# Optimization experiments

Hardware: AMD Instinct MI355X
Metric: run time of the kernel (lower is better)

The kernel has to match this reference:

```python
import jax, jax.numpy as jnp
import numpy as np

N_CLIN = 38
N_PIX = 36
N_NODES = N_CLIN + N_PIX  # 74
FV = 128
B = 1024
HID = 512
N_OUT = 1


def _base_edges():
    # Faithful to Network.get_edges: self-edges for all nodes, then for each
    # pixel node i, bidirectional edges to every clinical node.
    ids = np.arange(N_NODES)
    parts = [np.stack([ids, ids])]
    c = np.arange(N_CLIN)
    for i in range(N_CLIN, N_NODES):
        ii = np.full(N_CLIN, i)
        parts.append(np.stack([ii, c]))
        parts.append(np.stack([c, ii]))
    return np.concatenate(parts, axis=1)  # (2, 2810)


def setup_inputs() -> dict:
    key = jax.random.key(0)
    ks = jax.random.split(key, 10)
    base = _base_edges()  # (2, E0)
    # Batched edge index: per-sample copy offset by ind*N_NODES (batch-major order,
    # matching the torch.cat loop).
    offs = np.arange(B)[None, :, None] * N_NODES  # (1, B, 1)
    edge_index = (base[:, None, :] + offs).reshape(2, -1)  # (2, B*E0)
    s = 1.0 / np.sqrt(FV)
    return {
        "clinical_embeddings": jax.random.normal(ks[0], (B, N_CLIN, FV), jnp.float32),
        "image_embeddings": jax.random.normal(ks[1], (B, N_PIX, FV), jnp.float32),
        # RMRM graph-net params (single message-passing layer, fv_dim -> fv_dim)
        "W_self": jax.random.normal(ks[2], (FV, FV), jnp.float32) * s,
        "W_msg": jax.random.normal(ks[3], (FV, FV), jnp.float32) * s,
        "b_g": jnp.zeros((FV,), jnp.float32),
        # OutputBlock MLP params: fv_dim*(n_clinical+1)=4992 -> 512 -> 1
        "W1": jax.random.normal(ks[4], (FV * (N_CLIN + 1), HID), jnp.float32) * (1.0 / np.sqrt(FV * (N_CLIN + 1))),
        "b1": jnp.zeros((HID,), jnp.float32),
        "W2": jax.random.normal(ks[5], (HID, N_OUT), jnp.float32) * (1.0 / np.sqrt(HID)),
        "b2": jnp.zeros((N_OUT,), jnp.float32),
        "edge_index": jnp.asarray(edge_index, jnp.int32),
    }


def reference(clinical_embeddings, image_embeddings, W_self, W_msg, b_g, W1, b1, W2, b2, edge_index):
    # Assemble node features: [B, n_nodes, fv] -> flat [B*n_nodes, fv]
    x = jnp.concatenate([clinical_embeddings, image_embeddings], axis=1)
    x = x.reshape(-1, FV)
    src, dst = edge_index[0], edge_index[1]
    n_total = B * N_NODES
    # Mean-aggregated message passing (RMRM layer): gather + segment-sum
    msg = jax.ops.segment_sum(x[src], dst, num_segments=n_total)  # [B*N, FV]
    deg = jax.ops.segment_sum(jnp.ones_like(src, jnp.float32), dst, num_segments=n_total)
    agg = msg / deg[:, None]
    h = jax.nn.relu(x @ W_self + agg @ W_msg + b_g)  # [B*N, FV]
    h = h.reshape(B, N_NODES, FV)
    graph_fvs_c = h[:, :N_CLIN]          # [B, 38, FV]
    graph_fvs_i = h[:, N_CLIN:]          # [B, 36, FV]
    # AvgPool2d(6,6) over [B, FV, 6, 6] == mean over the 36 pixel nodes
    gap = graph_fvs_i.mean(axis=1)       # [B, FV]
    combined = jnp.concatenate([graph_fvs_c, gap[:, None, :]], axis=1).reshape(B, -1)
    # OutputBlock MLP
    out = jax.nn.relu(combined @ W1 + b1) @ W2 + b2  # [B, 1]
    return out
```

## Files before the change

### kernel.cpp

```cpp
#include <hip/hip_runtime.h>

#define FV 128
#define NCLIN 38
#define NPIX 36
#define NTOT 74
#define BATCH 1024
#define HID 512
#define COMB 4992
#define XPAD 136

typedef __attribute__((ext_vector_type(4))) float f32x4;
typedef __attribute__((ext_vector_type(8))) short s16x8;

#define WS_WCT  0
#define WS_WIT  8192
#define WS_COMB 16384
#define WS_W1T  2572288
#define WS_Z    3850240

__device__ __forceinline__ unsigned short bf16_rne(float f) {
    union { float f; unsigned int u; } v; v.f = f;
    unsigned int u = v.u;
    u += 0x7fffu + ((u >> 16) & 1u);
    return (unsigned short)(u >> 16);
}
__device__ __forceinline__ float bf2f(unsigned short h) {
    union { unsigned int u; float f; } v; v.u = ((unsigned int)h) << 16;
    return v.f;
}

__global__ __launch_bounds__(256) void k_static(
    const float* __restrict__ W1, const float* __restrict__ wself,
    const float* __restrict__ wmsg, float* __restrict__ ws)
{
    const int t = threadIdx.x;
    if (blockIdx.x == 78) {
        unsigned short* WcT = (unsigned short*)(ws + WS_WCT);
        unsigned short* WiT = (unsigned short*)(ws + WS_WIT);
        const int r  = blockIdx.y * 16 + (t >> 4);
        const int f0 = (t & 15) * 8;
#pragma unroll
        for (int j = 0; j < 8; ++j) {
            const int f = f0 + j;
            const int idx = r * 128 + f;
            const float wm = wmsg[idx];
            const float s  = wself[idx];
            WcT[f * 128 + r] = bf16_rne(s + wm * (1.0f / 37.0f));
            WiT[f * 128 + r] = bf16_rne(s + wm * (1.0f / 39.0f));
        }
        return;
    }
    unsigned short* W1T = (unsigned short*)(ws + WS_W1T);
    const int k0 = blockIdx.x * 64;
    const int n0 = blockIdx.y * 64;
    __shared__ float tile[64][65];
    const int r16 = t >> 4;
    const int c4  = (t & 15) * 4;
#pragma unroll
    for (int p = 0; p < 4; ++p) {
        const int r = p * 16 + r16;
        const float4 v = *(const float4*)&W1[(size_t)(k0 + r) * HID + n0 + c4];
        tile[r][c4 + 0] = v.x; tile[r][c4 + 1] = v.y;
        tile[r][c4 + 2] = v.z; tile[r][c4 + 3] = v.w;
    }
    __syncthreads();
    const int j  = t >> 2;
    const int i0 = (t & 3) * 16;
    unsigned short tmp[16];
#pragma unroll
    for (int s = 0; s < 16; ++s) tmp[s] = bf16_rne(tile[i0 + s][j]);
    unsigned short* dst = &W1T[(size_t)(n0 + j) * COMB + k0 + i0];
    *(uint4*)&dst[0] = *(uint4*)&tmp[0];
    *(uint4*)&dst[8] = *(uint4*)&tmp[8];
}

__global__ __launch_bounds__(256) void k_batch(
    const float* __restrict__ clin, const float* __restrict__ img,
    const float* __restrict__ wmsg, const float* __restrict__ bg,
    float* __restrict__ ws)
{
    const int b = blockIdx.x;
    const int t = threadIdx.x;

    __shared__ __align__(16) unsigned short xl[NTOT * XPAD];
    __shared__ float lc[128];
    __shared__ float li[128];
    __shared__ float tcv[128];
    __shared__ float tiv[128];

    const float* xc = clin + (size_t)b * NCLIN * FV;
    const float* xi = img  + (size_t)b * NPIX * FV;
    for (int i = t; i < NCLIN * 32; i += 256) {
        const int row = i >> 5, c4 = (i & 31) * 4;
        const float4 v = *(const float4*)&xc[row * 128 + c4];
        ushort4 u;
        u.x = bf16_rne(v.x); u.y = bf16_rne(v.y);
        u.z = bf16_rne(v.z); u.w = bf16_rne(v.w);
        *(ushort4*)&xl[row * XPAD + c4] = u;
    }
    for (int i = t; i < NPIX * 32; i += 256) {
        const int row = i >> 5, c4 = (i & 31) * 4;
        const float4 v = *(const float4*)&xi[row * 128 + c4];
        ushort4 u;
        u.x = bf16_rne(v.x); u.y = bf16_rne(v.y);
        u.z = bf16_rne(v.z); u.w = bf16_rne(v.w);
        *(ushort4*)&xl[(NCLIN + row) * XPAD + c4] = u;
    }
    __syncthreads();

    const int f = t & 127;
    if (t < 128) {
        float s = 0.f;
#pragma unroll
        for (int n = 0; n < NCLIN; ++n) s += bf2f(xl[n * XPAD + f]);
        lc[f] = s * (1.0f / 39.0f);
    } else {
        float s = 0.f;
#pragma unroll
        for (int n = 0; n < NPIX; ++n) s += bf2f(xl[(NCLIN + n) * XPAD + f]);
        li[f] = s * (1.0f / 37.0f);
    }
    __syncthreads();

    {
        const float* src = (t < 128) ? li : lc;
        float acc = bg[f];
#pragma unroll 4
        for (int k = 0; k < 128; ++k) acc += src[k] * wmsg[k * 128 + f];
        if (t < 128) tcv[f] = acc; else tiv[f] = acc;
    }
    __syncthreads();

    const unsigned short* WcT = (const unsigned short*)(ws + WS_WCT);
    const unsigned short* WiT = (const unsigned short*)(ws + WS_WIT);
    unsigned short* combined =
        (unsigned short*)(ws + WS_COMB) + (size_t)b * COMB;

    const int wave = t >> 6;
    const int lane = t & 63;
    const int l16  = lane & 15;
    const int q    = lane >> 4;
    const int n0   = wave * 32 + l16;

#pragma unroll
    for (int phase = 0; phase < 2; ++phase) {
        const int NN   = phase ? NPIX : NCLIN;
        const int xoff = phase ? NCLIN : 0;
        const unsigned short* WT = phase ? WiT : WcT;
        const float* tvv = phase ? tiv : tcv;

        const int r0 = xoff + ((l16      < NN) ? l16      : (NN - 1));
        const int r1 = xoff + ((16 + l16 < NN) ? 16 + l16 : (NN - 1));
        const int r2 = xoff + ((32 + l16 < NN) ? 32 + l16 : (NN - 1));

        f32x4 acc[3][2] = {};
#pragma unroll
        for (int kk = 0; kk < 4; ++kk) {
            const int ko = kk * 32 + q * 8;
            const s16x8 a0 = *(const s16x8*)&xl[r0 * XPAD + ko];
            const s16x8 a1 = *(const s16x8*)&xl[r1 * XPAD + ko];
            const s16x8 a2 = *(const s16x8*)&xl[r2 * XPAD + ko];
            const s16x8 b0 = *(const s16x8*)&WT[(n0)      * 128 + ko];
            const s16x8 b1 = *(const s16x8*)&WT[(n0 + 16) * 128 + ko];
            acc[0][0] = __builtin_amdgcn_mfma_f32_16x16x32_bf16(a0, b0, acc[0][0], 0, 0, 0);
            acc[0][1] = __builtin_amdgcn_mfma_f32_16x16x32_bf16(a0, b1, acc[0][1], 0, 0, 0);
            acc[1][0] = __builtin_amdgcn_mfma_f32_16x16x32_bf16(a1, b0, acc[1][0], 0, 0, 0);
            acc[1][1] = __builtin_amdgcn_mfma_f32_16x16x32_bf16(a1, b1, acc[1][1], 0, 0, 0);
            acc[2][0] = __builtin_amdgcn_mfma_f32_16x16x32_bf16(a2, b0, acc[2][0], 0, 0, 0);
            acc[2][1] = __builtin_amdgcn_mfma_f32_16x16x32_bf16(a2, b1, acc[2][1], 0, 0, 0);
        }

        const float t0 = tvv[wave * 32 + l16];
        const float t1 = tvv[wave * 32 + 16 + l16];

        if (phase == 0) {
#pragma unroll
            for (int rt = 0; rt < 3; ++rt) {
#pragma unroll
                for (int r = 0; r < 4; ++r) {
                    const int node = rt * 16 + q * 4 + r;
                    if (node < NCLIN) {
                        combined[node * 128 + wave * 32 + l16] =
                            bf16_rne(fmaxf(acc[rt][0][r] + t0, 0.f));
                        combined[node * 128 + wave * 32 + 16 + l16] =
                            bf16_rne(fmaxf(acc[rt][1][r] + t1, 0.f));
                    }
                }
            }
        } else {
            float g0 = 0.f, g1 = 0.f;
#pragma unroll
            for (int rt = 0; rt < 3; ++rt) {
#pragma unroll
                for (int r = 0; r < 4; ++r) {
                    const int node = rt * 16 + q * 4 + r;
                    if (node < NPIX) {
                        g0 += fmaxf(acc[rt][0][r] + t0, 0.f);
                        g1 += fmaxf(acc[rt][1][r] + t1, 0.f);
                    }
                }
            }
            g0 += __shfl_xor(g0, 16); g0 += __shfl_xor(g0, 32);
            g1 += __shfl_xor(g1, 16); g1 += __shfl_xor(g1, 32);
            if (q == 0) {
                combined[NCLIN * 128 + wave * 32 + l16] =
                    bf16_rne(g0 * (1.0f / 36.0f));
                combined[NCLIN * 128 + wave * 32 + 16 + l16] =
                    bf16_rne(g1 * (1.0f / 36.0f));
            }
        }
    }
}

__global__ __launch_bounds__(256) void k_gemm_mfma(float* __restrict__ ws)
{
    const unsigned short* Abase = (const unsigned short*)(ws + WS_COMB);
    const unsigned short* Bbase = (const unsigned short*)(ws + WS_W1T);
    const int m0    = blockIdx.x * 64;
    const int n0    = blockIdx.y * 64;
    const int ks    = blockIdx.z;
    const int kbase = ks * 1248;
    float* Z = ws + WS_Z + (size_t)ks * (BATCH * HID);

    __shared__ __align__(16) unsigned short As[64 * 40];
    __shared__ __align__(16) unsigned short Bs[64 * 40];

    const int t    = threadIdx.x;
    const int wave = t >> 6;
    const int lane = t & 63;
    const int wm   = (wave & 1) * 32;
    const int wn   = (wave >> 1) * 32;
    const int l16  = lane & 15;
    const int q    = lane >> 4;

    const int sr = t >> 2;
    const int sc = (t & 3) * 8;

    f32x4 acc00 = {}, acc01 = {}, acc10 = {}, acc11 = {};

    for (int kb = 0; kb < 1248; kb += 32) {
        __syncthreads();
        const int kk = kbase + kb + sc;
        *(uint4*)&As[sr * 40 + sc] =
            *(const uint4*)&Abase[(size_t)(m0 + sr) * COMB + kk];
        *(uint4*)&Bs[sr * 40 + sc] =
            *(const uint4*)&Bbase[(size_t)(n0 + sr) * COMB + kk];
        __syncthreads();

        const s16x8 a0 = *(const s16x8*)&As[(wm + l16) * 40 + q * 8];
        const s16x8 a1 = *(const s16x8*)&As[(wm + 16 + l16) * 40 + q * 8];
        const s16x8 b0 = *(const s16x8*)&Bs[(wn + l16) * 40 + q * 8];
        const s16x8 b1 = *(const s16x8*)&Bs[(wn + 16 + l16) * 40 + q * 8];

        acc00 = __builtin_amdgcn_mfma_f32_16x16x32_bf16(a0, b0, acc00, 0, 0, 0);
        acc01 = __builtin_amdgcn_mfma_f32_16x16x32_bf16(a0, b1, acc01, 0, 0, 0);
        acc10 = __builtin_amdgcn_mfma_f32_16x16x32_bf16(a1, b0, acc10, 0, 0, 0);
        acc11 = __builtin_amdgcn_mfma_f32_16x16x32_bf16(a1, b1, acc11, 0, 0, 0);
    }

    const int rbase = q * 4;
#pragma unroll
    for (int r = 0; r < 4; ++r) {
        const int mr0 = m0 + wm + rbase + r;
        Z[(size_t)(mr0)      * HID + n0 + wn +      l16] = acc00[r];
        Z[(size_t)(mr0)      * HID + n0 + wn + 16 + l16] = acc01[r];
        Z[(size_t)(mr0 + 16) * HID + n0 + wn +      l16] = acc10[r];
        Z[(size_t)(mr0 + 16) * HID + n0 + wn + 16 + l16] = acc11[r];
    }
}

__global__ __launch_bounds__(64) void k_out(
    const float* __restrict__ b1, const float* __restrict__ W2,
    const float* __restrict__ b2, const float* __restrict__ ws,
    float* __restrict__ out)
{
    const int b = blockIdx.x;
    const int l = threadIdx.x;
    const float* z0 = ws + WS_Z + (size_t)b * HID;
    const float* z1 = z0 + BATCH * HID;
    const float* z2 = z1 + BATCH * HID;
    const float* z3 = z2 + BATCH * HID;
    float s = 0.f;
#pragma unroll
    for (int j = 0; j < 8; ++j) {
        const int h = l + j * 64;
        float z = z0[h] + z1[h] + z2[h] + z3[h] + b1[h];
        z = fmaxf(z, 0.f);
        s += z * W2[h];
    }
#pragma unroll
    for (int off = 32; off > 0; off >>= 1) s += __shfl_down(s, off);
    if (l == 0) out[b] = s + b2[0];
}

extern "C" void kernel_launch(void* const* d_in, const int* in_sizes, int n_in,
                              void* d_out, int out_size, void* d_ws, size_t ws_size,
                              hipStream_t stream) {
    const float* clin  = (const float*)d_in[0];
    const float* img   = (const float*)d_in[1];
    const float* wself = (const float*)d_in[2];
    const float* wmsg  = (const float*)d_in[3];
    const float* bg    = (const float*)d_in[4];
    const float* W1    = (const float*)d_in[5];
    const float* b1    = (const float*)d_in[6];
    const float* W2    = (const float*)d_in[7];
    const float* b2    = (const float*)d_in[8];
    float* ws  = (float*)d_ws;
    float* out = (float*)d_out;

    k_static<<<dim3(79, 8), 256, 0, stream>>>(W1, wself, wmsg, ws);
    k_batch <<<dim3(BATCH), 256, 0, stream>>>(clin, img, wmsg, bg, ws);
    k_gemm_mfma<<<dim3(16, 8, 4), 256, 0, stream>>>(ws);
    k_out<<<dim3(BATCH), 64, 0, stream>>>(b1, W2, b2, ws, out);
}
```

Baseline: 160.0 us.

## Use MFMA for per-sample message projection and retile split-K GEMM

```diff
diff --git a/kernel.cpp b/kernel.cpp
--- a/kernel.cpp
+++ b/kernel.cpp
@@ -14,9 +14,11 @@
 
 #define WS_WCT  0
 #define WS_WIT  8192
-#define WS_COMB 16384
-#define WS_W1T  2572288
-#define WS_Z    3850240
+#define WS_WMT  16384
+#define WS_COMB 24576
+#define WS_W1T  2580480
+#define WS_Z    3858432
+#define ZSTRIDE (BATCH * HID)
 
 __device__ __forceinline__ unsigned short bf16_rne(float f) {
     union { float f; unsigned int u; } v; v.f = f;
@@ -37,6 +39,7 @@
     if (blockIdx.x == 78) {
         unsigned short* WcT = (unsigned short*)(ws + WS_WCT);
         unsigned short* WiT = (unsigned short*)(ws + WS_WIT);
+        unsigned short* WmT = (unsigned short*)(ws + WS_WMT);
         const int r  = blockIdx.y * 16 + (t >> 4);
         const int f0 = (t & 15) * 8;
 #pragma unroll
@@ -47,6 +50,7 @@
             const float s  = wself[idx];
             WcT[f * 128 + r] = bf16_rne(s + wm * (1.0f / 37.0f));
             WiT[f * 128 + r] = bf16_rne(s + wm * (1.0f / 39.0f));
+            WmT[f * 128 + r] = bf16_rne(wm);
         }
         return;
     }
@@ -76,15 +80,13 @@
 
 __global__ __launch_bounds__(256) void k_batch(
     const float* __restrict__ clin, const float* __restrict__ img,
-    const float* __restrict__ wmsg, const float* __restrict__ bg,
-    float* __restrict__ ws)
+    const float* __restrict__ bg, float* __restrict__ ws)
 {
     const int b = blockIdx.x;
     const int t = threadIdx.x;
 
     __shared__ __align__(16) unsigned short xl[NTOT * XPAD];
-    __shared__ float lc[128];
-    __shared__ float li[128];
+    __shared__ __align__(16) unsigned short sab[2 * 128];
     __shared__ float tcv[128];
     __shared__ float tiv[128];
 
@@ -113,34 +115,48 @@
         float s = 0.f;
 #pragma unroll
         for (int n = 0; n < NCLIN; ++n) s += bf2f(xl[n * XPAD + f]);
-        lc[f] = s * (1.0f / 39.0f);
+        sab[128 + f] = bf16_rne(s * (1.0f / 39.0f));
     } else {
         float s = 0.f;
 #pragma unroll
         for (int n = 0; n < NPIX; ++n) s += bf2f(xl[(NCLIN + n) * XPAD + f]);
-        li[f] = s * (1.0f / 37.0f);
+        sab[f] = bf16_rne(s * (1.0f / 37.0f));
     }
     __syncthreads();
-
-    {
-        const float* src = (t < 128) ? li : lc;
-        float acc = bg[f];
-#pragma unroll 4
-        for (int k = 0; k < 128; ++k) acc += src[k] * wmsg[k * 128 + f];
-        if (t < 128) tcv[f] = acc; else tiv[f] = acc;
-    }
-    __syncthreads();
-
-    const unsigned short* WcT = (const unsigned short*)(ws + WS_WCT);
-    const unsigned short* WiT = (const unsigned short*)(ws + WS_WIT);
-    unsigned short* combined =
-        (unsigned short*)(ws + WS_COMB) + (size_t)b * COMB;
 
     const int wave = t >> 6;
     const int lane = t & 63;
     const int l16  = lane & 15;
     const int q    = lane >> 4;
     const int n0   = wave * 32 + l16;
+
+    {
+        const unsigned short* WmT = (const unsigned short*)(ws + WS_WMT);
+        const int am = (l16 < 2) ? l16 : 0;
+        f32x4 ta = {}, tb = {};
+#pragma unroll
+        for (int kk = 0; kk < 4; ++kk) {
+            const int ko = kk * 32 + q * 8;
+            const s16x8 av  = *(const s16x8*)&sab[am * 128 + ko];
+            const s16x8 bv0 = *(const s16x8*)&WmT[(n0)      * 128 + ko];
+            const s16x8 bv1 = *(const s16x8*)&WmT[(n0 + 16) * 128 + ko];
+            ta = __builtin_amdgcn_mfma_f32_16x16x32_bf16(av, bv0, ta, 0, 0, 0);
+            tb = __builtin_amdgcn_mfma_f32_16x16x32_bf16(av, bv1, tb, 0, 0, 0);
+        }
+        if (q == 0) {
+            const int c0 = wave * 32 + l16;
+            const int c1 = c0 + 16;
+            const float bg0 = bg[c0], bg1 = bg[c1];
+            tcv[c0] = ta[0] + bg0;  tiv[c0] = ta[1] + bg0;
+            tcv[c1] = tb[0] + bg1;  tiv[c1] = tb[1] + bg1;
+        }
+    }
+    __syncthreads();
+
+    const unsigned short* WcT = (const unsigned short*)(ws + WS_WCT);
+    const unsigned short* WiT = (const unsigned short*)(ws + WS_WIT);
+    unsigned short* combined =
+        (unsigned short*)(ws + WS_COMB) + (size_t)b * COMB;
 
 #pragma unroll
     for (int phase = 0; phase < 2; ++phase) {
@@ -217,55 +233,71 @@
     const unsigned short* Abase = (const unsigned short*)(ws + WS_COMB);
     const unsigned short* Bbase = (const unsigned short*)(ws + WS_W1T);
     const int m0    = blockIdx.x * 64;
-    const int n0    = blockIdx.y * 64;
+    const int n0    = blockIdx.y * 128;
     const int ks    = blockIdx.z;
-    const int kbase = ks * 1248;
-    float* Z = ws + WS_Z + (size_t)ks * (BATCH * HID);
-
-    __shared__ __align__(16) unsigned short As[64 * 40];
-    __shared__ __align__(16) unsigned short Bs[64 * 40];
+    const int kbase = (ks < 4) ? 640 * ks : 2560 + 608 * (ks - 4);
+    const int kit   = (ks < 4) ? 20 : 19;
+    float* Z = ws + WS_Z + (size_t)ks * ZSTRIDE;
+
+    __shared__ __align__(16) unsigned short As[64 * 32];
+    __shared__ __align__(16) unsigned short Bs[128 * 32];
 
     const int t    = threadIdx.x;
     const int wave = t >> 6;
     const int lane = t & 63;
     const int wm   = (wave & 1) * 32;
-    const int wn   = (wave >> 1) * 32;
+    const int wn   = (wave >> 1) * 64;
     const int l16  = lane & 15;
     const int q    = lane >> 4;
 
-    const int sr = t >> 2;
-    const int sc = (t & 3) * 8;
-
-    f32x4 acc00 = {}, acc01 = {}, acc10 = {}, acc11 = {};
-
-    for (int kb = 0; kb < 1248; kb += 32) {
+    const int srow  = lane >> 2;
+    const int skoff = (lane & 3) * 8;
+    const unsigned short* gA =
+        Abase + (size_t)(m0 + wave * 16 + srow) * COMB + kbase + skoff;
+    const unsigned short* gB0 =
+        Bbase + (size_t)(n0 + wave * 32 + srow) * COMB + kbase + skoff;
+    const unsigned short* gB1 = gB0 + (size_t)16 * COMB;
+    unsigned short* lA  = As + wave * 512 + lane * 8;
+    unsigned short* lB0 = Bs + wave * 1024 + lane * 8;
+    unsigned short* lB1 = lB0 + 512;
+
+    f32x4 acc[2][4] = {};
+
+    for (int it = 0; it < kit; ++it) {
+        const int kk = it * 32;
         __syncthreads();
-        const int kk = kbase + kb + sc;
-        *(uint4*)&As[sr * 40 + sc] =
-            *(const uint4*)&Abase[(size_t)(m0 + sr) * COMB + kk];
-        *(uint4*)&Bs[sr * 40 + sc] =
-            *(const uint4*)&Bbase[(size_t)(n0 + sr) * COMB + kk];
+        *(uint4*)lA  = *(const uint4*)(gA  + kk);
+        *(uint4*)lB0 = *(const uint4*)(gB0 + kk);
+        *(uint4*)lB1 = *(const uint4*)(gB1 + kk);
         __syncthreads();
 
-        const s16x8 a0 = *(const s16x8*)&As[(wm + l16) * 40 + q * 8];
-        const s16x8 a1 = *(const s16x8*)&As[(wm + 16 + l16) * 40 + q * 8];
-        const s16x8 b0 = *(const s16x8*)&Bs[(wn + l16) * 40 + q * 8];
-        const s16x8 b1 = *(const s16x8*)&Bs[(wn + 16 + l16) * 40 + q * 8];
-
-        acc00 = __builtin_amdgcn_mfma_f32_16x16x32_bf16(a0, b0, acc00, 0, 0, 0);
-        acc01 = __builtin_amdgcn_mfma_f32_16x16x32_bf16(a0, b1, acc01, 0, 0, 0);
-        acc10 = __builtin_amdgcn_mfma_f32_16x16x32_bf16(a1, b0, acc10, 0, 0, 0);
-        acc11 = __builtin_amdgcn_mfma_f32_16x16x32_bf16(a1, b1, acc11, 0, 0, 0);
-    }
-
-    const int rbase = q * 4;
-#pragma unroll
-    for (int r = 0; r < 4; ++r) {
-        const int mr0 = m0 + wm + rbase + r;
-        Z[(size_t)(mr0)      * HID + n0 + wn +      l16] = acc00[r];
-        Z[(size_t)(mr0)      * HID + n0 + wn + 16 + l16] = acc01[r];
-        Z[(size_t)(mr0 + 16) * HID + n0 + wn +      l16] = acc10[r];
-        Z[(size_t)(mr0 + 16) * HID + n0 + wn + 16 + l16] = acc11[r];
+        const s16x8 a0 = *(const s16x8*)&As[(wm + l16)      * 32 + q * 8];
+        const s16x8 a1 = *(const s16x8*)&As[(wm + 16 + l16) * 32 + q * 8];
+        const s16x8 b0 = *(const s16x8*)&Bs[(wn + l16)      * 32 + q * 8];
+        const s16x8 b1 = *(const s16x8*)&Bs[(wn + 16 + l16) * 32 + q * 8];
+        const s16x8 b2 = *(const s16x8*)&Bs[(wn + 32 + l16) * 32 + q * 8];
+        const s16x8 b3 = *(const s16x8*)&Bs[(wn + 48 + l16) * 32 + q * 8];
+
+        acc[0][0] = __builtin_amdgcn_mfma_f32_16x16x32_bf16(a0, b0, acc[0][0], 0, 0, 0);
+        acc[0][1] = __builtin_amdgcn_mfma_f32_16x16x32_bf16(a0, b1, acc[0][1], 0, 0, 0);
+        acc[0][2] = __builtin_amdgcn_mfma_f32_16x16x32_bf16(a0, b2, acc[0][2], 0, 0, 0);
+        acc[0][3] = __builtin_amdgcn_mfma_f32_16x16x32_bf16(a0, b3, acc[0][3], 0, 0, 0);
+        acc[1][0] = __builtin_amdgcn_mfma_f32_16x16x32_bf16(a1, b0, acc[1][0], 0, 0, 0);
+        acc[1][1] = __builtin_amdgcn_mfma_f32_16x16x32_bf16(a1, b1, acc[1][1], 0, 0, 0);
+        acc[1][2] = __builtin_amdgcn_mfma_f32_16x16x32_bf16(a1, b2, acc[1][2], 0, 0, 0);
+        acc[1][3] = __builtin_amdgcn_mfma_f32_16x16x32_bf16(a1, b3, acc[1][3], 0, 0, 0);
+    }
+
+#pragma unroll
+    for (int a = 0; a < 2; ++a) {
+#pragma unroll
+        for (int r = 0; r < 4; ++r) {
+            const int mr = m0 + wm + 16 * a + q * 4 + r;
+#pragma unroll
+            for (int c = 0; c < 4; ++c) {
+                Z[(size_t)mr * HID + n0 + wn + 16 * c + l16] = acc[a][c][r];
+            }
+        }
     }
 }
 
@@ -276,17 +308,16 @@
 {
     const int b = blockIdx.x;
     const int l = threadIdx.x;
-    const float* z0 = ws + WS_Z + (size_t)b * HID;
-    const float* z1 = z0 + BATCH * HID;
-    const float* z2 = z1 + BATCH * HID;
-    const float* z3 = z2 + BATCH * HID;
+    const float* z = ws + WS_Z + (size_t)b * HID;
     float s = 0.f;
 #pragma unroll
     for (int j = 0; j < 8; ++j) {
         const int h = l + j * 64;
-        float z = z0[h] + z1[h] + z2[h] + z3[h] + b1[h];
-        z = fmaxf(z, 0.f);
-        s += z * W2[h];
+        float acc = b1[h];
+#pragma unroll
+        for (int p = 0; p < 8; ++p) acc += z[(size_t)p * ZSTRIDE + h];
+        acc = fmaxf(acc, 0.f);
+        s += acc * W2[h];
     }
 #pragma unroll
     for (int off = 32; off > 0; off >>= 1) s += __shfl_down(s, off);
@@ -309,7 +340,7 @@
     float* out = (float*)d_out;
 
     k_static<<<dim3(79, 8), 256, 0, stream>>>(W1, wself, wmsg, ws);
-    k_batch <<<dim3(BATCH), 256, 0, stream>>>(clin, img, wmsg, bg, ws);
-    k_gemm_mfma<<<dim3(16, 8, 4), 256, 0, stream>>>(ws);
+    k_batch <<<dim3(BATCH), 256, 0, stream>>>(clin, img, bg, ws);
+    k_gemm_mfma<<<dim3(16, 4, 8), 256, 0, stream>>>(ws);
     k_out<<<dim3(BATCH), 64, 0, stream>>>(b1, W2, b2, ws, out);
 }
```

After: 149.6 us. 1.07x faster.
